# Kernel tuning notes

Hardware: AMD Instinct MI355X
Metric: run time of the kernel (lower is better)

## Reference

```python
import jax, jax.numpy as jnp
import numpy as np

INPUT_DIM = 512
D_KQ = 64
D_V = 64
SEQ = 8192


def setup_inputs() -> dict:
    key = jax.random.key(0)
    k_x, k_q, k_k, k_v = jax.random.split(key, 4)
    x = jax.random.normal(k_x, (SEQ, INPUT_DIM), dtype=jnp.float32)
    # Original uses torch.rand (uniform [0,1)) for the parameters.
    W_query = jax.random.uniform(k_q, (INPUT_DIM, D_KQ), dtype=jnp.float32)
    W_key = jax.random.uniform(k_k, (INPUT_DIM, D_KQ), dtype=jnp.float32)
    W_value = jax.random.uniform(k_v, (INPUT_DIM, D_V), dtype=jnp.float32)
    return {"x": x, "W_query": W_query, "W_key": W_key, "W_value": W_value}


def reference(x, W_query, W_key, W_value):
    # Full-recompute path of AttentionOptimized: single-head attention.
    Q = x @ W_query          # [T, d_kq]
    K = x @ W_key            # [T, d_kq]
    V = x @ W_value          # [T, d_v]
    scale = jnp.asarray(D_KQ, x.dtype) ** 0.5
    scores = Q @ K.T         # [T, T]
    attn = jax.nn.softmax(scores / scale, axis=-1)
    return attn @ V          # [T, d_v]
```

## Files before the change

### kernel.cpp

```cpp
#include <hip/hip_runtime.h>
#include <hip/hip_bf16.h>
#include <math.h>

#define SEQ 8192
#define DIN 512
#define DH  64
#define SG  8
#define CHUNK (SEQ / SG)
#define BK  64
#define NIT (CHUNK / BK)
#define LDK 64
#define SXP 516

typedef float f32x4 __attribute__((ext_vector_type(4)));
typedef short short8 __attribute__((ext_vector_type(8)));
typedef ushort us4 __attribute__((ext_vector_type(4)));

static __device__ __forceinline__ ushort bf16_of(float v) {
  __hip_bfloat16 h = __float2bfloat16(v);
  return *reinterpret_cast<ushort*>(&h);
}
static __device__ __forceinline__ float f_of_bf16(ushort u) {
  __hip_bfloat16 h;
  *reinterpret_cast<ushort*>(&h) = u;
  return __bfloat162float(h);
}
static __device__ __forceinline__ f32x4 mfma16(short8 a, short8 b, f32x4 c) {
  return __builtin_amdgcn_mfma_f32_16x16x32_bf16(a, b, c, 0, 0, 0);
}
static __device__ __forceinline__ uint pack_bf16(float a, float b) {
  __hip_bfloat162 h2 = __float22bfloat162_rn(make_float2(a, b));
  return *reinterpret_cast<uint*>(&h2);
}
static __device__ __forceinline__ int slot_of(int p) {
  return ((((p >> 2) & 1) * 2 + (p >> 5)) << 4) | (((p >> 3) & 3) << 2) | (p & 3);
}
static __device__ __forceinline__ int swz(int row, int col) {
  return col ^ ((row & 7) << 3);
}

static __device__ __forceinline__ void bar_lgkm() {
  asm volatile("s_waitcnt lgkmcnt(0)" ::: "memory");
  __builtin_amdgcn_s_barrier();
}

__global__ __launch_bounds__(256, 2) void pgemm_kernel(
    const float* __restrict__ x,  const float* __restrict__ Wq,
    const float* __restrict__ Wk, const float* __restrict__ Wv,
    ushort* __restrict__ Qh, ushort* __restrict__ Ql,
    ushort* __restrict__ Kh, ushort* __restrict__ Kl,
    ushort* __restrict__ Vt) {
  __shared__ float sx[16][SXP];
  float* mb = &sx[0][0];

  const int tid = threadIdx.x;
  const int wv = tid >> 6, lane = tid & 63;
  const int ln = lane & 15, qd = lane >> 4;
  const int rb = blockIdx.x * 16;

  {
    const float4* xg = reinterpret_cast<const float4*>(x + (size_t)rb * DIN);
#pragma unroll
    for (int j = 0; j < 8; ++j) {
      const int idx = tid + 256 * j;
      const int row = idx >> 7;
      const int col = (idx & 127) * 4;
      *reinterpret_cast<float4*>(&sx[row][col]) = xg[idx];
    }
  }
  __syncthreads();

  f32x4 acc[3][4];
#pragma unroll
  for (int m = 0; m < 3; ++m)
#pragma unroll
    for (int nt = 0; nt < 4; ++nt)
#pragma unroll
      for (int i = 0; i < 4; ++i) acc[m][nt][i] = 0.f;

  const int kb = wv * 128;
  const int wbase = (kb + qd * 8) * 64 + ln;

  float wf[2][32];
#define LDW(kt_, m_, buf_)                                                     \
  do {                                                                         \
    const float* W_ = ((m_) == 0) ? Wq : (((m_) == 1) ? Wk : Wv);              \
    const int o_ = wbase + (kt_) * 32 * 64;                                    \
    _Pragma("unroll") for (int nt = 0; nt < 4; ++nt)                           \
      _Pragma("unroll") for (int j = 0; j < 8; ++j)                            \
        wf[buf_][nt * 8 + j] = W_[o_ + j * 64 + nt * 16];                      \
  } while (0)

  LDW(0, 0, 0);
#pragma unroll
  for (int kt = 0; kt < 4; ++kt) {
    const int k0 = kb + kt * 32;
    float xs[8];
    *reinterpret_cast<float4*>(xs) =
        *reinterpret_cast<const float4*>(&sx[ln][k0 + qd * 8]);
    *reinterpret_cast<float4*>(xs + 4) =
        *reinterpret_cast<const float4*>(&sx[ln][k0 + qd * 8 + 4]);
    ushort ah[8] __attribute__((aligned(16)));
    ushort al[8] __attribute__((aligned(16)));
#pragma unroll
    for (int j = 0; j < 8; ++j) {
      const ushort h = bf16_of(xs[j]);
      ah[j] = h;
      al[j] = bf16_of(xs[j] - f_of_bf16(h));
    }
    const short8 Ah = *reinterpret_cast<short8*>(ah);
    const short8 Al = *reinterpret_cast<short8*>(al);
#pragma unroll
    for (int m = 0; m < 3; ++m) {
      const int g = kt * 3 + m;
      const int buf = g & 1;
      if (g < 11) {
        const int gn = g + 1;
        LDW(gn / 3, gn % 3, buf ^ 1);
      }
      const float scale = (m == 0) ? 0.125f * 1.44269504088896f : 1.0f;
#pragma unroll
      for (int nt = 0; nt < 4; ++nt) {
        ushort bh8[8] __attribute__((aligned(16)));
        ushort bl8[8] __attribute__((aligned(16)));
#pragma unroll
        for (int j = 0; j < 8; ++j) {
          const float v = wf[buf][nt * 8 + j] * scale;
          const ushort h = bf16_of(v);
          bh8[j] = h;
          bl8[j] = bf16_of(v - f_of_bf16(h));
        }
        const short8 bh = *reinterpret_cast<short8*>(bh8);
        const short8 bl = *reinterpret_cast<short8*>(bl8);
        acc[m][nt] = mfma16(Ah, bh, acc[m][nt]);
        acc[m][nt] = mfma16(Ah, bl, acc[m][nt]);
        acc[m][nt] = mfma16(Al, bh, acc[m][nt]);
      }
    }
  }
#undef LDW

  const int eidx = (qd * 4) * 64 + ln;
  __syncthreads();
  if (wv >= 2) {
    float* b = mb + (size_t)(wv - 2) * 3072;
#pragma unroll
    for (int m = 0; m < 3; ++m)
#pragma unroll
      for (int nt = 0; nt < 4; ++nt)
#pragma unroll
        for (int r = 0; r < 4; ++r)
          b[m * 1024 + eidx + r * 64 + nt * 16] = acc[m][nt][r];
  }
  __syncthreads();
  if (wv < 2) {
    const float* b = mb + (size_t)wv * 3072;
#pragma unroll
    for (int m = 0; m < 3; ++m)
#pragma unroll
      for (int nt = 0; nt < 4; ++nt)
#pragma unroll
        for (int r = 0; r < 4; ++r)
          acc[m][nt][r] += b[m * 1024 + eidx + r * 64 + nt * 16];
  }
  __syncthreads();
  if (wv == 1) {
#pragma unroll
    for (int m = 0; m < 3; ++m)
#pragma unroll
      for (int nt = 0; nt < 4; ++nt)
#pragma unroll
        for (int r = 0; r < 4; ++r)
          mb[m * 1024 + eidx + r * 64 + nt * 16] = acc[m][nt][r];
  }
  __syncthreads();
  if (wv == 0) {
#pragma unroll
    for (int m = 0; m < 3; ++m)
#pragma unroll
      for (int nt = 0; nt < 4; ++nt)
#pragma unroll
        for (int r = 0; r < 4; ++r)
          acc[m][nt][r] += mb[m * 1024 + eidx + r * 64 + nt * 16];

#pragma unroll
    for (int m = 0; m < 2; ++m) {
      ushort* H = (m == 0) ? Qh : Kh;
      ushort* L = (m == 0) ? Ql : Kl;
#pragma unroll
      for (int nt = 0; nt < 4; ++nt)
#pragma unroll
        for (int r = 0; r < 4; ++r) {
          const float v = acc[m][nt][r];
          const int row = rb + qd * 4 + r;
          const int col = nt * 16 + ln;
          const ushort h = bf16_of(v);
          H[(size_t)row * DH + col] = h;
          L[(size_t)row * DH + col] = bf16_of(v - f_of_bf16(h));
        }
    }
#pragma unroll
    for (int nt = 0; nt < 4; ++nt) {
      ushort vp[4] __attribute__((aligned(8)));
#pragma unroll
      for (int r = 0; r < 4; ++r) vp[r] = bf16_of(acc[2][nt][r]);
      *reinterpret_cast<us4*>(Vt + (size_t)(nt * 16 + ln) * SEQ + rb + qd * 4) =
          *reinterpret_cast<us4*>(vp);
    }
  }
}

__global__ __launch_bounds__(256, 2) void flash_kernel(
    const ushort* __restrict__ Qh, const ushort* __restrict__ Ql,
    const ushort* __restrict__ Kh, const ushort* __restrict__ Kl,
    const ushort* __restrict__ Vt,
    ushort* __restrict__ Opart, float* __restrict__ Mpart,
    float* __restrict__ Lpart) {
  __shared__ __attribute__((aligned(16))) ushort sKh[3][BK][LDK];
  __shared__ __attribute__((aligned(16))) ushort sKl[3][BK][LDK];
  __shared__ __attribute__((aligned(16))) ushort sVt[3][DH][LDK];

  const int tid  = threadIdx.x;
  const int wv   = tid >> 6;
  const int lane = tid & 63;
  const int ln   = lane & 15;
  const int qd   = lane >> 4;
  const int bid  = blockIdx.x;
  const int sg   = bid & (SG - 1);
  const int qt   = bid >> 3;
  const int qrow0  = qt * 128 + wv * 32;
  const int k0base = sg * CHUNK;

  const int r0 = tid >> 3, g0 = (tid & 7) * 8;
  const int r1 = r0 + 32,  g1 = g0;
  const int sr0 = slot_of(r0), sr1 = slot_of(r1);

  const ushort one_u = (ln == 0) ? (ushort)0x3F80 : (ushort)0;
  short8 afr1;
#pragma unroll
  for (int j = 0; j < 8; ++j) afr1[j] = (short)one_u;

  short8 bqh[2][2], bql[2][2];
#pragma unroll
  for (int s = 0; s < 2; ++s)
#pragma unroll
    for (int kt = 0; kt < 2; ++kt) {
      bqh[s][kt] = *reinterpret_cast<const short8*>(
          Qh + (size_t)(qrow0 + s * 16 + ln) * DH + kt * 32 + qd * 8);
      bql[s][kt] = *reinterpret_cast<const short8*>(
          Ql + (size_t)(qrow0 + s * 16 + ln) * DH + kt * 32 + qd * 8);
    }

  f32x4 accO[2][4], accL[2];
  float m_run[2] = {-INFINITY, -INFINITY};
#pragma unroll
  for (int s = 0; s < 2; ++s) {
#pragma unroll
    for (int nt = 0; nt < 4; ++nt)
#pragma unroll
      for (int i = 0; i < 4; ++i) accO[s][nt][i] = 0.f;
#pragma unroll
    for (int i = 0; i < 4; ++i) accL[s][i] = 0.f;
  }
  const f32x4 z4 = {0.f, 0.f, 0.f, 0.f};

  f32x4 accSA[2][4], accSB[2][4];

  uint4 pk0, pk1, pl0, pl1, pv0, pv1;
#define LOAD_TILES(k0_)                                                        \
  do {                                                                         \
    pk0 = *reinterpret_cast<const uint4*>(Kh + (size_t)((k0_) + r0) * DH + g0);\
    pk1 = *reinterpret_cast<const uint4*>(Kh + (size_t)((k0_) + r1) * DH + g1);\
    pl0 = *reinterpret_cast<const uint4*>(Kl + (size_t)((k0_) + r0) * DH + g0);\
    pl1 = *reinterpret_cast<const uint4*>(Kl + (size_t)((k0_) + r1) * DH + g1);\
    pv0 = *reinterpret_cast<const uint4*>(Vt + (size_t)r0 * SEQ + (k0_) + g0); \
    pv1 = *reinterpret_cast<const uint4*>(Vt + (size_t)r1 * SEQ + (k0_) + g1); \
  } while (0)
#define STORE_TILES(b_)                                                        \
  do {                                                                         \
    *reinterpret_cast<uint4*>(&sKh[b_][sr0][swz(sr0, g0)]) = pk0;              \
    *reinterpret_cast<uint4*>(&sKh[b_][sr1][swz(sr1, g1)]) = pk1;              \
    *reinterpret_cast<uint4*>(&sKl[b_][sr0][swz(sr0, g0)]) = pl0;              \
    *reinterpret_cast<uint4*>(&sKl[b_][sr1][swz(sr1, g1)]) = pl1;              \
    *reinterpret_cast<uint4*>(&sVt[b_][r0][swz(r0, g0)])   = pv0;              \
    *reinterpret_cast<uint4*>(&sVt[b_][r1][swz(r1, g1)])   = pv1;              \
  } while (0)

#define QK_PHASE(ACC, b_)                                                      \
  do {                                                                         \
    _Pragma("unroll") for (int nt = 0; nt < 4; ++nt) {                         \
      const int kr = nt * 16 + ln;                                             \
      const short8 kh0 = *reinterpret_cast<const short8*>(                     \
          &sKh[b_][kr][swz(kr, qd * 8)]);                                      \
      const short8 kh1 = *reinterpret_cast<const short8*>(                     \
          &sKh[b_][kr][swz(kr, 32 + qd * 8)]);                                 \
      const short8 kl0 = *reinterpret_cast<const short8*>(                     \
          &sKl[b_][kr][swz(kr, qd * 8)]);                                      \
      const short8 kl1 = *reinterpret_cast<const short8*>(                     \
          &sKl[b_][kr][swz(kr, 32 + qd * 8)]);                                 \
      _Pragma("unroll") for (int s = 0; s < 2; ++s) {                          \
        ACC[s][nt] = mfma16(kh0, bqh[s][0], z4);                               \
        ACC[s][nt] = mfma16(kh1, bqh[s][1], ACC[s][nt]);                       \
        ACC[s][nt] = mfma16(kh0, bql[s][0], ACC[s][nt]);                       \
        ACC[s][nt] = mfma16(kh1, bql[s][1], ACC[s][nt]);                       \
        ACC[s][nt] = mfma16(kl0, bqh[s][0], ACC[s][nt]);                       \
        ACC[s][nt] = mfma16(kl1, bqh[s][1], ACC[s][nt]);                       \
      }                                                                        \
    }                                                                          \
  } while (0)

#define SMPV_PHASE(ACC, bc_)                                                   \
  do {                                                                         \
    uint pkd[2][4][2];                                                         \
    _Pragma("unroll") for (int s = 0; s < 2; ++s) {                            \
      float tmax = fmaxf(fmaxf(ACC[s][0][0], ACC[s][0][1]), ACC[s][0][2]);     \
      tmax = fmaxf(fmaxf(tmax, ACC[s][0][3]), ACC[s][1][0]);                   \
      tmax = fmaxf(fmaxf(tmax, ACC[s][1][1]), ACC[s][1][2]);                   \
      tmax = fmaxf(fmaxf(tmax, ACC[s][1][3]), ACC[s][2][0]);                   \
      tmax = fmaxf(fmaxf(tmax, ACC[s][2][1]), ACC[s][2][2]);                   \
      tmax = fmaxf(fmaxf(tmax, ACC[s][2][3]), ACC[s][3][0]);                   \
      tmax = fmaxf(fmaxf(tmax, ACC[s][3][1]), ACC[s][3][2]);                   \
      tmax = fmaxf(tmax, ACC[s][3][3]);                                        \
      tmax = fmaxf(tmax, __shfl_xor(tmax, 16));                                \
      tmax = fmaxf(tmax, __shfl_xor(tmax, 32));                                \
      if (tmax > m_run[s] + 8.f) {       \
        const float mnew  = fmaxf(m_run[s], tmax);                             \
        const float alpha = exp2f(m_run[s] - mnew);                            \
        m_run[s] = mnew;                                                       \
        _Pragma("unroll") for (int nt = 0; nt < 4; ++nt)                       \
          _Pragma("unroll") for (int i = 0; i < 4; ++i)                        \
            accO[s][nt][i] *= alpha;                                           \
        accL[s][0] *= alpha;                                                   \
      }                                                                        \
      const float mr = m_run[s];                                               \
      _Pragma("unroll") for (int nt = 0; nt < 4; ++nt) {                       \
        pkd[s][nt][0] = pack_bf16(exp2f(ACC[s][nt][0] - mr),                   \
                                  exp2f(ACC[s][nt][1] - mr));                  \
        pkd[s][nt][1] = pack_bf16(exp2f(ACC[s][nt][2] - mr),                   \
                                  exp2f(ACC[s][nt][3] - mr));                  \
      }                                                                        \
    }                                                                          \
    _Pragma("unroll") for (int kt2 = 0; kt2 < 2; ++kt2) {                      \
      short8 pfrag[2];                                                         \
      _Pragma("unroll") for (int s = 0; s < 2; ++s) {                          \
        uint4 du;                                                              \
        du.x = pkd[s][kt2][0];                                                 \
        du.y = pkd[s][kt2][1];                                                 \
        du.z = pkd[s][kt2 + 2][0];                                             \
        du.w = pkd[s][kt2 + 2][1];                                             \
        pfrag[s] = *reinterpret_cast<short8*>(&du);                            \
      }                                                                        \
      _Pragma("unroll") for (int nt2 = 0; nt2 < 4; ++nt2) {                    \
        const int vr = nt2 * 16 + ln;                                          \
        const short8 vA = *reinterpret_cast<const short8*>(                    \
            &sVt[bc_][vr][swz(vr, kt2 * 32 + qd * 8)]);                        \
        accO[0][nt2] = mfma16(vA, pfrag[0], accO[0][nt2]);                     \
        accO[1][nt2] = mfma16(vA, pfrag[1], accO[1][nt2]);                     \
      }                                                                        \
      accL[0] = mfma16(afr1, pfrag[0], accL[0]);                               \
      accL[1] = mfma16(afr1, pfrag[1], accL[1]);                               \
    }                                                                          \
  } while (0)

  LOAD_TILES(k0base);
  STORE_TILES(0);
  LOAD_TILES(k0base + BK);
  STORE_TILES(1);
  LOAD_TILES(k0base + 2 * BK);
  bar_lgkm();
  QK_PHASE(accSA, 0);

#define BODY(t_, AC, AN)                                                       \
  do {                                                                         \
    if ((t_) <= NIT - 3) STORE_TILES(((t_) + 2) % 3);                          \
    if ((t_) <= NIT - 4) LOAD_TILES(k0base + ((t_) + 3) * BK);                 \
    if ((t_) <= NIT - 2) QK_PHASE(AN, ((t_) + 1) % 3);                         \
    SMPV_PHASE(AC, (t_) % 3);                                                  \
    if ((t_) <= NIT - 2) bar_lgkm();                                           \
  } while (0)

  BODY(0,  accSA, accSB);
  BODY(1,  accSB, accSA);
  BODY(2,  accSA, accSB);
  BODY(3,  accSB, accSA);
  BODY(4,  accSA, accSB);
  BODY(5,  accSB, accSA);
  BODY(6,  accSA, accSB);
  BODY(7,  accSB, accSA);
  BODY(8,  accSA, accSB);
  BODY(9,  accSB, accSA);
  BODY(10, accSA, accSB);
  BODY(11, accSB, accSA);
  BODY(12, accSA, accSB);
  BODY(13, accSB, accSA);
  BODY(14, accSA, accSB);
  BODY(15, accSB, accSA);
#undef BODY
#undef QK_PHASE
#undef SMPV_PHASE
#undef LOAD_TILES
#undef STORE_TILES

#pragma unroll
  for (int s = 0; s < 2; ++s) {
    const int qrow = qrow0 + s * 16 + ln;
    ushort* Ob = Opart + ((size_t)sg * SEQ + qrow) * DH;
#pragma unroll
    for (int nt = 0; nt < 4; ++nt) {
      ushort op[4] __attribute__((aligned(8)));
#pragma unroll
      for (int r = 0; r < 4; ++r) op[r] = bf16_of(accO[s][nt][r]);
      *reinterpret_cast<us4*>(Ob + nt * 16 + qd * 4) =
          *reinterpret_cast<us4*>(op);
    }
    if (qd == 0) {
      Mpart[(size_t)sg * SEQ + qrow] = m_run[s];
      Lpart[(size_t)sg * SEQ + qrow] = accL[s][0];
    }
  }
}

__global__ __launch_bounds__(256) void merge_kernel(
    const ushort* __restrict__ Opart, const float* __restrict__ Mpart,
    const float* __restrict__ Lpart, float* __restrict__ out) {
  const int idx = blockIdx.x * 256 + threadIdx.x;
  const int row = idx >> 4;
  const int c4  = (idx & 15) * 4;

  float m[SG];
  float M = -INFINITY;
#pragma unroll
  for (int i = 0; i < SG; ++i) {
    m[i] = Mpart[(size_t)i * SEQ + row];
    M = fmaxf(M, m[i]);
  }
  float L = 0.f;
  float a0 = 0.f, a1 = 0.f, a2 = 0.f, a3 = 0.f;
#pragma unroll
  for (int i = 0; i < SG; ++i) {
    const float w = exp2f(m[i] - M);
    L += w * Lpart[(size_t)i * SEQ + row];
    const us4 o = *reinterpret_cast<const us4*>(
        Opart + ((size_t)i * SEQ + row) * DH + c4);
    a0 += w * f_of_bf16(o[0]);
    a1 += w * f_of_bf16(o[1]);
    a2 += w * f_of_bf16(o[2]);
    a3 += w * f_of_bf16(o[3]);
  }
  const float rL = 1.0f / L;
  float4 res = make_float4(a0 * rL, a1 * rL, a2 * rL, a3 * rL);
  *reinterpret_cast<float4*>(out + (size_t)row * DH + c4) = res;
}

extern "C" void kernel_launch(void* const* d_in, const int* in_sizes, int n_in,
                              void* d_out, int out_size, void* d_ws, size_t ws_size,
                              hipStream_t stream) {
  const float* x  = (const float*)d_in[0];
  const float* Wq = (const float*)d_in[1];
  const float* Wk = (const float*)d_in[2];
  const float* Wv = (const float*)d_in[3];
  float* out = (float*)d_out;

  const size_t S64 = (size_t)SEQ * DH;
  ushort* Qh = (ushort*)d_ws;
  ushort* Ql = Qh + S64;
  ushort* Kh = Ql + S64;
  ushort* Kl = Kh + S64;
  ushort* Vt = Kl + S64;
  ushort* Op = Vt + S64;
  float*  Mp = (float*)(Op + (size_t)SG * S64);
  float*  Lp = Mp + (size_t)SG * SEQ;

  pgemm_kernel<<<SEQ / 16, 256, 0, stream>>>(x, Wq, Wk, Wv, Qh, Ql, Kh, Kl, Vt);
  flash_kernel<<<(SEQ / 128) * SG, 256, 0, stream>>>(Qh, Ql, Kh, Kl, Vt, Op, Mp, Lp);
  merge_kernel<<<(SEQ * 16) / 256, 256, 0, stream>>>(Op, Mp, Lp, out);
}
```

Baseline: 129.7 us.

## Fuse projection, flash, and merge kernels into one cooperative launch with grid syncs

Turns the three kernels into device phases that share one LDS buffer, and runs them in a single cooperative kernel of 512 blocks with grid-wide syncs between phases. The aim is to remove the launch overhead and tail gaps between the three dispatches. If the cooperative launch fails, it falls back to the original three launches. All 512 blocks must be co-resident (2 per CU at 72KB LDS), and the grid barriers add their own cost and can hurt occupancy.

```diff
diff --git a/kernel.cpp b/kernel.cpp
--- a/kernel.cpp
+++ b/kernel.cpp
@@ -1,6 +1,9 @@
 #include <hip/hip_runtime.h>
+#include <hip/hip_cooperative_groups.h>
 #include <hip/hip_bf16.h>
 #include <math.h>
+
+namespace cg = cooperative_groups;
 
 #define SEQ 8192
 #define DIN 512
@@ -11,6 +14,7 @@
 #define NIT (CHUNK / BK)
 #define LDK 64
 #define SXP 516
+#define SMEM_BYTES 73728
 
 typedef float f32x4 __attribute__((ext_vector_type(4)));
 typedef short short8 __attribute__((ext_vector_type(8)));
@@ -38,20 +42,20 @@
 static __device__ __forceinline__ int swz(int row, int col) {
   return col ^ ((row & 7) << 3);
 }
-
 static __device__ __forceinline__ void bar_lgkm() {
   asm volatile("s_waitcnt lgkmcnt(0)" ::: "memory");
   __builtin_amdgcn_s_barrier();
 }
 
-__global__ __launch_bounds__(256, 2) void pgemm_kernel(
+static __device__ void pgemm_phase(
+    char* smem,
     const float* __restrict__ x,  const float* __restrict__ Wq,
     const float* __restrict__ Wk, const float* __restrict__ Wv,
     ushort* __restrict__ Qh, ushort* __restrict__ Ql,
     ushort* __restrict__ Kh, ushort* __restrict__ Kl,
     ushort* __restrict__ Vt) {
-  __shared__ float sx[16][SXP];
-  float* mb = &sx[0][0];
+  float (*sx)[SXP] = reinterpret_cast<float (*)[SXP]>(smem);
+  float* mb = reinterpret_cast<float*>(smem);
 
   const int tid = threadIdx.x;
   const int wv = tid >> 6, lane = tid & 63;
@@ -210,15 +214,16 @@
   }
 }
 
-__global__ __launch_bounds__(256, 2) void flash_kernel(
+static __device__ void flash_phase(
+    char* smem,
     const ushort* __restrict__ Qh, const ushort* __restrict__ Ql,
     const ushort* __restrict__ Kh, const ushort* __restrict__ Kl,
     const ushort* __restrict__ Vt,
     ushort* __restrict__ Opart, float* __restrict__ Mpart,
     float* __restrict__ Lpart) {
-  __shared__ __attribute__((aligned(16))) ushort sKh[3][BK][LDK];
-  __shared__ __attribute__((aligned(16))) ushort sKl[3][BK][LDK];
-  __shared__ __attribute__((aligned(16))) ushort sVt[3][DH][LDK];
+  ushort (*sKh)[BK][LDK] = reinterpret_cast<ushort (*)[BK][LDK]>(smem);
+  ushort (*sKl)[BK][LDK] = reinterpret_cast<ushort (*)[BK][LDK]>(smem + 24576);
+  ushort (*sVt)[DH][LDK] = reinterpret_cast<ushort (*)[DH][LDK]>(smem + 49152);
 
   const int tid  = threadIdx.x;
   const int wv   = tid >> 6;
@@ -420,7 +425,7 @@
   }
 }
 
-__global__ __launch_bounds__(256) void merge_kernel(
+static __device__ void merge_phase(
     const ushort* __restrict__ Opart, const float* __restrict__ Mpart,
     const float* __restrict__ Lpart, float* __restrict__ out) {
   const int idx = blockIdx.x * 256 + threadIdx.x;
@@ -452,6 +457,51 @@
   *reinterpret_cast<float4*>(out + (size_t)row * DH + c4) = res;
 }
 
+__global__ __launch_bounds__(256, 2) void fused_kernel(
+    const float* __restrict__ x,  const float* __restrict__ Wq,
+    const float* __restrict__ Wk, const float* __restrict__ Wv,
+    ushort* __restrict__ Qh, ushort* __restrict__ Ql,
+    ushort* __restrict__ Kh, ushort* __restrict__ Kl,
+    ushort* __restrict__ Vt, ushort* __restrict__ Op,
+    float* __restrict__ Mp, float* __restrict__ Lp,
+    float* __restrict__ out) {
+  __shared__ __attribute__((aligned(16))) char smem[SMEM_BYTES];
+
+  pgemm_phase(smem, x, Wq, Wk, Wv, Qh, Ql, Kh, Kl, Vt);
+  __threadfence();
+  cg::this_grid().sync();
+  flash_phase(smem, Qh, Ql, Kh, Kl, Vt, Op, Mp, Lp);
+  __threadfence();
+  cg::this_grid().sync();
+  merge_phase(Op, Mp, Lp, out);
+}
+
+__global__ __launch_bounds__(256, 2) void pgemm_kernel(
+    const float* __restrict__ x,  const float* __restrict__ Wq,
+    const float* __restrict__ Wk, const float* __restrict__ Wv,
+    ushort* __restrict__ Qh, ushort* __restrict__ Ql,
+    ushort* __restrict__ Kh, ushort* __restrict__ Kl,
+    ushort* __restrict__ Vt) {
+  __shared__ __attribute__((aligned(16))) char smem[16 * SXP * 4];
+  pgemm_phase(smem, x, Wq, Wk, Wv, Qh, Ql, Kh, Kl, Vt);
+}
+
+__global__ __launch_bounds__(256, 2) void flash_kernel(
+    const ushort* __restrict__ Qh, const ushort* __restrict__ Ql,
+    const ushort* __restrict__ Kh, const ushort* __restrict__ Kl,
+    const ushort* __restrict__ Vt,
+    ushort* __restrict__ Opart, float* __restrict__ Mpart,
+    float* __restrict__ Lpart) {
+  __shared__ __attribute__((aligned(16))) char smem[SMEM_BYTES];
+  flash_phase(smem, Qh, Ql, Kh, Kl, Vt, Opart, Mpart, Lpart);
+}
+
+__global__ __launch_bounds__(256) void merge_kernel(
+    const ushort* __restrict__ Opart, const float* __restrict__ Mpart,
+    const float* __restrict__ Lpart, float* __restrict__ out) {
+  merge_phase(Opart, Mpart, Lpart, out);
+}
+
 extern "C" void kernel_launch(void* const* d_in, const int* in_sizes, int n_in,
                               void* d_out, int out_size, void* d_ws, size_t ws_size,
                               hipStream_t stream) {
@@ -471,7 +521,16 @@
   float*  Mp = (float*)(Op + (size_t)SG * S64);
   float*  Lp = Mp + (size_t)SG * SEQ;
 
-  pgemm_kernel<<<SEQ / 16, 256, 0, stream>>>(x, Wq, Wk, Wv, Qh, Ql, Kh, Kl, Vt);
-  flash_kernel<<<(SEQ / 128) * SG, 256, 0, stream>>>(Qh, Ql, Kh, Kl, Vt, Op, Mp, Lp);
-  merge_kernel<<<(SEQ * 16) / 256, 256, 0, stream>>>(Op, Mp, Lp, out);
-}
+  void* args[] = {(void*)&x,  (void*)&Wq, (void*)&Wk, (void*)&Wv,
+                  (void*)&Qh, (void*)&Ql, (void*)&Kh, (void*)&Kl,
+                  (void*)&Vt, (void*)&Op, (void*)&Mp, (void*)&Lp,
+                  (void*)&out};
+  const hipError_t e = hipLaunchCooperativeKernel(
+      reinterpret_cast<void*>(fused_kernel), dim3(512), dim3(256), args, 0,
+      stream);
+  if (e != hipSuccess) {
+    pgemm_kernel<<<SEQ / 16, 256, 0, stream>>>(x, Wq, Wk, Wv, Qh, Ql, Kh, Kl, Vt);
+    flash_kernel<<<(SEQ / 128) * SG, 256, 0, stream>>>(Qh, Ql, Kh, Kl, Vt, Op, Mp, Lp);
+    merge_kernel<<<(SEQ * 16) / 256, 256, 0, stream>>>(Op, Mp, Lp, out);
+  }
+}
```

New measurement: 460.6 us. 3.55x slower.

## Fuse split-K merge into flash kernel via last-block atomic counter

Applied to the files above, without the earlier changes.

Removes the separate merge kernel. Each flash block increments a per-query-tile global counter after writing its partial results, and the last of the SG blocks for that tile does the log-sum-exp merge and writes the final output. This drops one kernel launch and lets merging overlap with other tiles' attention work, at the cost of threadfences, an atomic, and a serialized tail in the last block. The counter is never reset but is tested modulo SG, so it stays correct across repeated calls.

```diff
diff --git a/kernel.cpp b/kernel.cpp
--- a/kernel.cpp
+++ b/kernel.cpp
@@ -16,6 +16,8 @@
 typedef short short8 __attribute__((ext_vector_type(8)));
 typedef ushort us4 __attribute__((ext_vector_type(4)));
 
+__device__ uint g_cnt[SEQ / 128];
+
 static __device__ __forceinline__ ushort bf16_of(float v) {
   __hip_bfloat16 h = __float2bfloat16(v);
   return *reinterpret_cast<ushort*>(&h);
@@ -38,7 +40,6 @@
 static __device__ __forceinline__ int swz(int row, int col) {
   return col ^ ((row & 7) << 3);
 }
-
 static __device__ __forceinline__ void bar_lgkm() {
   asm volatile("s_waitcnt lgkmcnt(0)" ::: "memory");
   __builtin_amdgcn_s_barrier();
@@ -215,10 +216,11 @@
     const ushort* __restrict__ Kh, const ushort* __restrict__ Kl,
     const ushort* __restrict__ Vt,
     ushort* __restrict__ Opart, float* __restrict__ Mpart,
-    float* __restrict__ Lpart) {
+    float* __restrict__ Lpart, float* __restrict__ out) {
   __shared__ __attribute__((aligned(16))) ushort sKh[3][BK][LDK];
   __shared__ __attribute__((aligned(16))) ushort sKl[3][BK][LDK];
   __shared__ __attribute__((aligned(16))) ushort sVt[3][DH][LDK];
+  __shared__ int sLast;
 
   const int tid  = threadIdx.x;
   const int wv   = tid >> 6;
@@ -418,38 +420,44 @@
       Lpart[(size_t)sg * SEQ + qrow] = accL[s][0];
     }
   }
-}
-
-__global__ __launch_bounds__(256) void merge_kernel(
-    const ushort* __restrict__ Opart, const float* __restrict__ Mpart,
-    const float* __restrict__ Lpart, float* __restrict__ out) {
-  const int idx = blockIdx.x * 256 + threadIdx.x;
-  const int row = idx >> 4;
-  const int c4  = (idx & 15) * 4;
-
-  float m[SG];
-  float M = -INFINITY;
-#pragma unroll
-  for (int i = 0; i < SG; ++i) {
-    m[i] = Mpart[(size_t)i * SEQ + row];
-    M = fmaxf(M, m[i]);
-  }
-  float L = 0.f;
-  float a0 = 0.f, a1 = 0.f, a2 = 0.f, a3 = 0.f;
-#pragma unroll
-  for (int i = 0; i < SG; ++i) {
-    const float w = exp2f(m[i] - M);
-    L += w * Lpart[(size_t)i * SEQ + row];
-    const us4 o = *reinterpret_cast<const us4*>(
-        Opart + ((size_t)i * SEQ + row) * DH + c4);
-    a0 += w * f_of_bf16(o[0]);
-    a1 += w * f_of_bf16(o[1]);
-    a2 += w * f_of_bf16(o[2]);
-    a3 += w * f_of_bf16(o[3]);
-  }
-  const float rL = 1.0f / L;
-  float4 res = make_float4(a0 * rL, a1 * rL, a2 * rL, a3 * rL);
-  *reinterpret_cast<float4*>(out + (size_t)row * DH + c4) = res;
+
+  __threadfence();
+  __syncthreads();
+  if (tid == 0) {
+    const uint old = atomicAdd(&g_cnt[qt], 1u);
+    sLast = ((old & (SG - 1)) == (SG - 1)) ? 1 : 0;
+  }
+  __syncthreads();
+  if (sLast) {
+    __threadfence();
+    for (int i = tid; i < 128 * 16; i += 256) {
+      const int row = qt * 128 + (i >> 4);
+      const int c4  = (i & 15) * 4;
+      float mv[SG];
+      float M = -INFINITY;
+#pragma unroll
+      for (int p = 0; p < SG; ++p) {
+        mv[p] = Mpart[(size_t)p * SEQ + row];
+        M = fmaxf(M, mv[p]);
+      }
+      float L = 0.f;
+      float a0 = 0.f, a1 = 0.f, a2 = 0.f, a3 = 0.f;
+#pragma unroll
+      for (int p = 0; p < SG; ++p) {
+        const float w = exp2f(mv[p] - M);
+        L += w * Lpart[(size_t)p * SEQ + row];
+        const us4 o = *reinterpret_cast<const us4*>(
+            Opart + ((size_t)p * SEQ + row) * DH + c4);
+        a0 += w * f_of_bf16(o[0]);
+        a1 += w * f_of_bf16(o[1]);
+        a2 += w * f_of_bf16(o[2]);
+        a3 += w * f_of_bf16(o[3]);
+      }
+      const float rL = 1.0f / L;
+      float4 res = make_float4(a0 * rL, a1 * rL, a2 * rL, a3 * rL);
+      *reinterpret_cast<float4*>(out + (size_t)row * DH + c4) = res;
+    }
+  }
 }
 
 extern "C" void kernel_launch(void* const* d_in, const int* in_sizes, int n_in,
@@ -472,6 +480,6 @@
   float*  Lp = Mp + (size_t)SG * SEQ;
 
   pgemm_kernel<<<SEQ / 16, 256, 0, stream>>>(x, Wq, Wk, Wv, Qh, Ql, Kh, Kl, Vt);
-  flash_kernel<<<(SEQ / 128) * SG, 256, 0, stream>>>(Qh, Ql, Kh, Kl, Vt, Op, Mp, Lp);
-  merge_kernel<<<(SEQ * 16) / 256, 256, 0, stream>>>(Op, Mp, Lp, out);
-}
+  flash_kernel<<<(SEQ / 128) * SG, 256, 0, stream>>>(Qh, Ql, Kh, Kl, Vt, Op, Mp,
+                                                     Lp, out);
+}
```

Result: slower. 213.6 us (+64.8%).

## Switch attention to fp16 MFMA and drop K low-part split

Applied to the files above, without the earlier changes.

Moves Q, K, V, P and partial outputs from bf16 to fp16. fp16's extra mantissa bits allow dropping the K low-order correction term, so QK now uses 4 MFMAs per tile instead of 6. This also removes the Kl buffer, its global loads and its LDS tiles. It adds s_setprio around the MFMA phases to favour matrix issue. The cost is fp16 range risk: scores, exp values and V must stay within fp16 limits, and the pack uses round-toward-zero conversion.

```diff
diff --git a/kernel.cpp b/kernel.cpp
--- a/kernel.cpp
+++ b/kernel.cpp
@@ -15,6 +15,8 @@
 typedef float f32x4 __attribute__((ext_vector_type(4)));
 typedef short short8 __attribute__((ext_vector_type(8)));
 typedef ushort us4 __attribute__((ext_vector_type(4)));
+typedef _Float16 half8 __attribute__((ext_vector_type(8)));
+typedef __fp16 fp16x2 __attribute__((ext_vector_type(2)));
 
 static __device__ __forceinline__ ushort bf16_of(float v) {
   __hip_bfloat16 h = __float2bfloat16(v);
@@ -28,9 +30,21 @@
 static __device__ __forceinline__ f32x4 mfma16(short8 a, short8 b, f32x4 c) {
   return __builtin_amdgcn_mfma_f32_16x16x32_bf16(a, b, c, 0, 0, 0);
 }
-static __device__ __forceinline__ uint pack_bf16(float a, float b) {
-  __hip_bfloat162 h2 = __float22bfloat162_rn(make_float2(a, b));
-  return *reinterpret_cast<uint*>(&h2);
+static __device__ __forceinline__ ushort f16b(float v) {
+  _Float16 h = (_Float16)v;
+  return *reinterpret_cast<ushort*>(&h);
+}
+static __device__ __forceinline__ float f_of_f16(ushort u) {
+  _Float16 h = *reinterpret_cast<_Float16*>(&u);
+  return (float)h;
+}
+static __device__ __forceinline__ f32x4 mfma16f(short8 a, short8 b, f32x4 c) {
+  return __builtin_amdgcn_mfma_f32_16x16x32_f16(
+      __builtin_bit_cast(half8, a), __builtin_bit_cast(half8, b), c, 0, 0, 0);
+}
+static __device__ __forceinline__ uint pack_f16(float a, float b) {
+  fp16x2 h = __builtin_amdgcn_cvt_pkrtz(a, b);
+  return __builtin_bit_cast(uint, h);
 }
 static __device__ __forceinline__ int slot_of(int p) {
   return ((((p >> 2) & 1) * 2 + (p >> 5)) << 4) | (((p >> 3) & 3) << 2) | (p & 3);
@@ -38,7 +52,6 @@
 static __device__ __forceinline__ int swz(int row, int col) {
   return col ^ ((row & 7) << 3);
 }
-
 static __device__ __forceinline__ void bar_lgkm() {
   asm volatile("s_waitcnt lgkmcnt(0)" ::: "memory");
   __builtin_amdgcn_s_barrier();
@@ -48,8 +61,7 @@
     const float* __restrict__ x,  const float* __restrict__ Wq,
     const float* __restrict__ Wk, const float* __restrict__ Wv,
     ushort* __restrict__ Qh, ushort* __restrict__ Ql,
-    ushort* __restrict__ Kh, ushort* __restrict__ Kl,
-    ushort* __restrict__ Vt) {
+    ushort* __restrict__ Kh, ushort* __restrict__ Vt) {
   __shared__ float sx[16][SXP];
   float* mb = &sx[0][0];
 
@@ -184,26 +196,22 @@
           acc[m][nt][r] += mb[m * 1024 + eidx + r * 64 + nt * 16];
 
 #pragma unroll
-    for (int m = 0; m < 2; ++m) {
-      ushort* H = (m == 0) ? Qh : Kh;
-      ushort* L = (m == 0) ? Ql : Kl;
-#pragma unroll
-      for (int nt = 0; nt < 4; ++nt)
-#pragma unroll
-        for (int r = 0; r < 4; ++r) {
-          const float v = acc[m][nt][r];
-          const int row = rb + qd * 4 + r;
-          const int col = nt * 16 + ln;
-          const ushort h = bf16_of(v);
-          H[(size_t)row * DH + col] = h;
-          L[(size_t)row * DH + col] = bf16_of(v - f_of_bf16(h));
-        }
-    }
+    for (int nt = 0; nt < 4; ++nt)
+#pragma unroll
+      for (int r = 0; r < 4; ++r) {
+        const int row = rb + qd * 4 + r;
+        const int col = nt * 16 + ln;
+        const float vq = acc[0][nt][r];
+        const ushort qh = f16b(vq);
+        Qh[(size_t)row * DH + col] = qh;
+        Ql[(size_t)row * DH + col] = f16b(vq - f_of_f16(qh));
+        Kh[(size_t)row * DH + col] = f16b(acc[1][nt][r]);
+      }
 #pragma unroll
     for (int nt = 0; nt < 4; ++nt) {
       ushort vp[4] __attribute__((aligned(8)));
 #pragma unroll
-      for (int r = 0; r < 4; ++r) vp[r] = bf16_of(acc[2][nt][r]);
+      for (int r = 0; r < 4; ++r) vp[r] = f16b(acc[2][nt][r]);
       *reinterpret_cast<us4*>(Vt + (size_t)(nt * 16 + ln) * SEQ + rb + qd * 4) =
           *reinterpret_cast<us4*>(vp);
     }
@@ -212,12 +220,10 @@
 
 __global__ __launch_bounds__(256, 2) void flash_kernel(
     const ushort* __restrict__ Qh, const ushort* __restrict__ Ql,
-    const ushort* __restrict__ Kh, const ushort* __restrict__ Kl,
-    const ushort* __restrict__ Vt,
+    const ushort* __restrict__ Kh, const ushort* __restrict__ Vt,
     ushort* __restrict__ Opart, float* __restrict__ Mpart,
     float* __restrict__ Lpart) {
   __shared__ __attribute__((aligned(16))) ushort sKh[3][BK][LDK];
-  __shared__ __attribute__((aligned(16))) ushort sKl[3][BK][LDK];
   __shared__ __attribute__((aligned(16))) ushort sVt[3][DH][LDK];
 
   const int tid  = threadIdx.x;
@@ -235,7 +241,7 @@
   const int r1 = r0 + 32,  g1 = g0;
   const int sr0 = slot_of(r0), sr1 = slot_of(r1);
 
-  const ushort one_u = (ln == 0) ? (ushort)0x3F80 : (ushort)0;
+  const ushort one_u = (ln == 0) ? (ushort)0x3C00 : (ushort)0;
   short8 afr1;
 #pragma unroll
   for (int j = 0; j < 8; ++j) afr1[j] = (short)one_u;
@@ -266,13 +272,11 @@
 
   f32x4 accSA[2][4], accSB[2][4];
 
-  uint4 pk0, pk1, pl0, pl1, pv0, pv1;
+  uint4 pk0, pk1, pv0, pv1;
 #define LOAD_TILES(k0_)                                                        \
   do {                                                                         \
     pk0 = *reinterpret_cast<const uint4*>(Kh + (size_t)((k0_) + r0) * DH + g0);\
     pk1 = *reinterpret_cast<const uint4*>(Kh + (size_t)((k0_) + r1) * DH + g1);\
-    pl0 = *reinterpret_cast<const uint4*>(Kl + (size_t)((k0_) + r0) * DH + g0);\
-    pl1 = *reinterpret_cast<const uint4*>(Kl + (size_t)((k0_) + r1) * DH + g1);\
     pv0 = *reinterpret_cast<const uint4*>(Vt + (size_t)r0 * SEQ + (k0_) + g0); \
     pv1 = *reinterpret_cast<const uint4*>(Vt + (size_t)r1 * SEQ + (k0_) + g1); \
   } while (0)
@@ -280,33 +284,27 @@
   do {                                                                         \
     *reinterpret_cast<uint4*>(&sKh[b_][sr0][swz(sr0, g0)]) = pk0;              \
     *reinterpret_cast<uint4*>(&sKh[b_][sr1][swz(sr1, g1)]) = pk1;              \
-    *reinterpret_cast<uint4*>(&sKl[b_][sr0][swz(sr0, g0)]) = pl0;              \
-    *reinterpret_cast<uint4*>(&sKl[b_][sr1][swz(sr1, g1)]) = pl1;              \
     *reinterpret_cast<uint4*>(&sVt[b_][r0][swz(r0, g0)])   = pv0;              \
     *reinterpret_cast<uint4*>(&sVt[b_][r1][swz(r1, g1)])   = pv1;              \
   } while (0)
 
 #define QK_PHASE(ACC, b_)                                                      \
   do {                                                                         \
+    __builtin_amdgcn_s_setprio(1);                                             \
     _Pragma("unroll") for (int nt = 0; nt < 4; ++nt) {                         \
       const int kr = nt * 16 + ln;                                             \
       const short8 kh0 = *reinterpret_cast<const short8*>(                     \
           &sKh[b_][kr][swz(kr, qd * 8)]);                                      \
       const short8 kh1 = *reinterpret_cast<const short8*>(                     \
           &sKh[b_][kr][swz(kr, 32 + qd * 8)]);                                 \
-      const short8 kl0 = *reinterpret_cast<const short8*>(                     \
-          &sKl[b_][kr][swz(kr, qd * 8)]);                                      \
-      const short8 kl1 = *reinterpret_cast<const short8*>(                     \
-          &sKl[b_][kr][swz(kr, 32 + qd * 8)]);                                 \
       _Pragma("unroll") for (int s = 0; s < 2; ++s) {                          \
-        ACC[s][nt] = mfma16(kh0, bqh[s][0], z4);                               \
-        ACC[s][nt] = mfma16(kh1, bqh[s][1], ACC[s][nt]);                       \
-        ACC[s][nt] = mfma16(kh0, bql[s][0], ACC[s][nt]);                       \
-        ACC[s][nt] = mfma16(kh1, bql[s][1], ACC[s][nt]);                       \
-        ACC[s][nt] = mfma16(kl0, bqh[s][0], ACC[s][nt]);                       \
-        ACC[s][nt] = mfma16(kl1, bqh[s][1], ACC[s][nt]);                       \
+        ACC[s][nt] = mfma16f(kh0, bqh[s][0], z4);                              \
+        ACC[s][nt] = mfma16f(kh1, bqh[s][1], ACC[s][nt]);                      \
+        ACC[s][nt] = mfma16f(kh0, bql[s][0], ACC[s][nt]);                      \
+        ACC[s][nt] = mfma16f(kh1, bql[s][1], ACC[s][nt]);                      \
       }                                                                        \
     }                                                                          \
+    __builtin_amdgcn_s_setprio(0);                                             \
   } while (0)
 
 #define SMPV_PHASE(ACC, bc_)                                                   \
@@ -334,12 +332,13 @@
       }                                                                        \
       const float mr = m_run[s];                                               \
       _Pragma("unroll") for (int nt = 0; nt < 4; ++nt) {                       \
-        pkd[s][nt][0] = pack_bf16(exp2f(ACC[s][nt][0] - mr),                   \
-                                  exp2f(ACC[s][nt][1] - mr));                  \
-        pkd[s][nt][1] = pack_bf16(exp2f(ACC[s][nt][2] - mr),                   \
-                                  exp2f(ACC[s][nt][3] - mr));                  \
+        pkd[s][nt][0] = pack_f16(exp2f(ACC[s][nt][0] - mr),                    \
+                                 exp2f(ACC[s][nt][1] - mr));                   \
+        pkd[s][nt][1] = pack_f16(exp2f(ACC[s][nt][2] - mr),                    \
+                                 exp2f(ACC[s][nt][3] - mr));                   \
       }                                                                        \
     }                                                                          \
+    __builtin_amdgcn_s_setprio(1);                                             \
     _Pragma("unroll") for (int kt2 = 0; kt2 < 2; ++kt2) {                      \
       short8 pfrag[2];                                                         \
       _Pragma("unroll") for (int s = 0; s < 2; ++s) {                          \
@@ -354,12 +353,13 @@
         const int vr = nt2 * 16 + ln;                                          \
         const short8 vA = *reinterpret_cast<const short8*>(                    \
             &sVt[bc_][vr][swz(vr, kt2 * 32 + qd * 8)]);                        \
-        accO[0][nt2] = mfma16(vA, pfrag[0], accO[0][nt2]);                     \
-        accO[1][nt2] = mfma16(vA, pfrag[1], accO[1][nt2]);                     \
+        accO[0][nt2] = mfma16f(vA, pfrag[0], accO[0][nt2]);                    \
+        accO[1][nt2] = mfma16f(vA, pfrag[1], accO[1][nt2]);                    \
       }                                                                        \
-      accL[0] = mfma16(afr1, pfrag[0], accL[0]);                               \
-      accL[1] = mfma16(afr1, pfrag[1], accL[1]);                               \
+      accL[0] = mfma16f(afr1, pfrag[0], accL[0]);                              \
+      accL[1] = mfma16f(afr1, pfrag[1], accL[1]);                              \
     }                                                                          \
+    __builtin_amdgcn_s_setprio(0);                                             \
   } while (0)
 
   LOAD_TILES(k0base);
@@ -409,7 +409,7 @@
     for (int nt = 0; nt < 4; ++nt) {
       ushort op[4] __attribute__((aligned(8)));
 #pragma unroll
-      for (int r = 0; r < 4; ++r) op[r] = bf16_of(accO[s][nt][r]);
+      for (int r = 0; r < 4; ++r) op[r] = f16b(accO[s][nt][r]);
       *reinterpret_cast<us4*>(Ob + nt * 16 + qd * 4) =
           *reinterpret_cast<us4*>(op);
     }
@@ -442,10 +442,10 @@
     L += w * Lpart[(size_t)i * SEQ + row];
     const us4 o = *reinterpret_cast<const us4*>(
         Opart + ((size_t)i * SEQ + row) * DH + c4);
-    a0 += w * f_of_bf16(o[0]);
-    a1 += w * f_of_bf16(o[1]);
-    a2 += w * f_of_bf16(o[2]);
-    a3 += w * f_of_bf16(o[3]);
+    a0 += w * f_of_f16(o[0]);
+    a1 += w * f_of_f16(o[1]);
+    a2 += w * f_of_f16(o[2]);
+    a3 += w * f_of_f16(o[3]);
   }
   const float rL = 1.0f / L;
   float4 res = make_float4(a0 * rL, a1 * rL, a2 * rL, a3 * rL);
@@ -465,13 +465,12 @@
   ushort* Qh = (ushort*)d_ws;
   ushort* Ql = Qh + S64;
   ushort* Kh = Ql + S64;
-  ushort* Kl = Kh + S64;
-  ushort* Vt = Kl + S64;
+  ushort* Vt = Kh + S64;
   ushort* Op = Vt + S64;
   float*  Mp = (float*)(Op + (size_t)SG * S64);
   float*  Lp = Mp + (size_t)SG * SEQ;
 
-  pgemm_kernel<<<SEQ / 16, 256, 0, stream>>>(x, Wq, Wk, Wv, Qh, Ql, Kh, Kl, Vt);
-  flash_kernel<<<(SEQ / 128) * SG, 256, 0, stream>>>(Qh, Ql, Kh, Kl, Vt, Op, Mp, Lp);
+  pgemm_kernel<<<SEQ / 16, 256, 0, stream>>>(x, Wq, Wk, Wv, Qh, Ql, Kh, Vt);
+  flash_kernel<<<(SEQ / 128) * SG, 256, 0, stream>>>(Qh, Ql, Kh, Vt, Op, Mp, Lp);
   merge_kernel<<<(SEQ * 16) / 256, 256, 0, stream>>>(Op, Mp, Lp, out);
 }
```

New measurement: 123.0 us (median of 2 runs). 1.05x faster.
